# Performance work log

Measured on AMD Instinct MI355X. Metric: run time of the kernel, lower is better.

The kernel has to match this reference:

```python
import jax, jax.numpy as jnp
from jax import lax
import numpy as np

K = 3  # kernel size per dim, dimension=6 -> 3**6 = 729 taps
OFFS = np.stack(np.meshgrid(*([np.arange(K)] * 6), indexing='ij'), axis=-1).reshape(-1, 6).astype(np.int32)


def conv6d(x, kernel):
    """Dense emulation of a 1->1 channel MinkowskiConvolution over 6 spatial dims.

    x: (b, s, s, d, d, d, d) with zeros at absent sparse coordinates.
    kernel: (729,) flattened 3^6 kernel (in=out=1 channel, no bias).
    Zeros at absent coordinates contribute nothing to the gathered sums, so the
    dense conv equals the sparse conv evaluated everywhere.
    """
    xp = jnp.pad(x, [(0, 0)] + [(1, 1)] * 6)
    offs = jnp.asarray(OFFS)
    zero = jnp.int32(0)

    def body(acc, ow):
        off, wt = ow
        sl = lax.dynamic_slice(
            xp, (zero, off[0], off[1], off[2], off[3], off[4], off[5]), x.shape)
        return acc + wt * sl, None

    acc, _ = lax.scan(jax.checkpoint(body), jnp.zeros_like(x), (offs, kernel))
    return acc


def _transpose6d(t):
    # swap the two scale dims and the two image-coordinate pairs:
    # (b, s1, s2, h1, w1, h2, w2) -> (b, s2, s1, h2, w2, h1, w1)
    return jnp.transpose(t, (0, 2, 1, 5, 6, 3, 4))


def setup_inputs() -> dict:
    key = jax.random.key(0)
    k1, k2 = jax.random.split(key)
    x = jax.random.normal(k1, (1, 2, 2, 32, 32, 32, 32), dtype=jnp.float32)
    kernel = jax.random.normal(k2, (K ** 6,), dtype=jnp.float32) * 0.05
    return {"x": x, "kernel": kernel}


def reference(x, kernel):
    # MinkowskiConvolution outputs at the input coordinate set; MinkowskiSigmoid
    # acts on features at those coordinates; to_dense() zero-fills elsewhere.
    # Dense equivalent: mask to the input nonzero set.
    mask = (x != 0).astype(x.dtype)
    branch = lambda z: jax.nn.sigmoid(conv6d(jax.nn.relu(z), kernel))
    # symmetric mode: conv(x) + T(conv(T(x))); T(coords(T(x))) == coords(x)
    y = mask * (branch(x) + _transpose6d(branch(_transpose6d(x))))
    b, s1, s2, d1, d2, d3, d4 = y.shape
    y = y.reshape(b, s1 * s2, d1, d2, d3, d4).sum(axis=1)  # (b, h1, w1, h2, w2)
    return y
```

## Files before the change

kernel.cpp:

```cpp
#include <hip/hip_runtime.h>

typedef _Float16 half8 __attribute__((ext_vector_type(8)));
typedef float f16v __attribute__((ext_vector_type(16)));
typedef float f4 __attribute__((ext_vector_type(4)));
typedef unsigned long long ull;

#define X_SLAB   1048576
#define PLANE_BYTES (34*36*4*2)
#define RPT_SITES (34*34*34*36)
#define RPT_OFF  65536
#define RPT_SLACK 4096
#define TAB_N    (3*6*3*512)
#define TAB_ELEMS  (4*81*8)

__global__ __launch_bounds__(256)
void prep(const float* __restrict__ x, const float* __restrict__ w,
          ull* __restrict__ rpt, _Float16* __restrict__ tabm) {
    unsigned s = blockIdx.x * 256 + threadIdx.x;
    if (s < RPT_SITES) {
        unsigned q = s;
        int j4 = q % 36; q /= 36;
        int j3 = q % 34; q /= 34;
        int j2 = q % 34; q /= 34;
        int j1 = q;
        union { _Float16 h[4]; ull u; } pk;
        pk.u = 0ull;
        if (j1 >= 1 && j1 <= 32 && j2 >= 1 && j2 <= 32 &&
            j3 >= 1 && j3 <= 32 && j4 >= 1 && j4 <= 32) {
            size_t off = (size_t)(j1-1)*32768 + (j2-1)*1024 + (j3-1)*32 + (j4-1);
            #pragma unroll
            for (int t = 0; t < 4; ++t)
                pk.h[t] = (_Float16)fmaxf(x[(size_t)t*X_SLAB + off], 0.f);
        }
        rpt[s] = pk.u;
    }
    if (blockIdx.x == 0) {
        for (int idx = threadIdx.x; idx < TAB_N; idx += 256) {
            int j = idx & 7, l = (idx >> 3) & 63, slice = idx >> 9;
            int p4 = slice % 3, j2rel = (slice/3) % 6, p2 = slice/18;
            int n32 = l & 31;
            int d2 = n32 >> 3, n8 = n32 & 7;
            int k = 8*(l>>5) + j;
            int p5h = k >> 2, t = k & 3;
            int p3 = j2rel - d2;
            float val = 0.f;
            if (p5h < 3 && p3 >= 0 && p3 <= 2) {
                int br = n8 & 1, sc = n8 >> 1, s1 = sc >> 1, s2 = sc & 1;
                int t1 = t >> 1, t2 = t & 1;
                int a = t1 - s1 + 1, b = t2 - s2 + 1;
                int widx = (br == 0)
                    ? (a*243 + b*81 + p2*27 + p3*9 + p4*3 + p5h)
                    : (b*243 + a*81 + p4*27 + p5h*9 + p2*3 + p3);
                val = w[widx];
            }
            tabm[idx] = (_Float16)val;
        }
    }
}

__global__ __launch_bounds__(256)
void conv_mfma(const float* __restrict__ x, const ull* __restrict__ rpt,
               const _Float16* __restrict__ tabm, float* __restrict__ out) {
    __shared__ unsigned char msk[2048];

    const int tid  = threadIdx.x;
    const int lane = tid & 63;
    const int wv   = tid >> 6;
    const int e2b  = blockIdx.x * 4;
    const int e1   = blockIdx.y;
    const int bz   = blockIdx.z;
    const size_t pbase = (size_t)e1*32768 + (size_t)e2b*1024 + (size_t)bz*512;

    {
        int p0 = tid * 8;
        int d2 = p0 >> 9, rem = p0 & 511;
        const float* xb = x + pbase + (size_t)d2*1024 + rem;
        #pragma unroll
        for (int g = 0; g < 2; ++g) {
            f4 a0 = *(const f4*)(xb + (size_t)0*X_SLAB + 4*g);
            f4 a1 = *(const f4*)(xb + (size_t)1*X_SLAB + 4*g);
            f4 a2 = *(const f4*)(xb + (size_t)2*X_SLAB + 4*g);
            f4 a3 = *(const f4*)(xb + (size_t)3*X_SLAB + 4*g);
            unsigned wbits = 0;
            #pragma unroll
            for (int q = 0; q < 4; ++q) {
                unsigned b = (a0[q] != 0.f ? 1u : 0u) | (a1[q] != 0.f ? 2u : 0u)
                           | (a2[q] != 0.f ? 4u : 0u) | (a3[q] != 0.f ? 8u : 0u);
                wbits |= b << (8*q);
            }
            *(unsigned*)&msk[p0 + 4*g] = wbits;
        }
    }
    __syncthreads();

    f16v acc[4];
    #pragma unroll
    for (int r = 0; r < 4; ++r)
        #pragma unroll
        for (int i = 0; i < 16; ++i) acc[r][i] = 0.f;

    const int R   = bz*16 + wv*4;
    const int j4b = (lane & 31) + 2*(lane >> 5);
    const char* awave = (const char*)rpt + (size_t)(R*36 + j4b)*8;

    #pragma unroll 1
    for (int p2 = 0; p2 < 3; ++p2) {
        #pragma unroll 2
        for (int j2 = 0; j2 < 6; ++j2) {
            const int it = p2*6 + j2;
            const char* aptr = awave + ((size_t)(e1+p2)*34 + (e2b+j2))*PLANE_BYTES;
            const _Float16* tb = tabm + it*1536 + lane*8;
            half8 B0 = *(const half8*)(tb);
            half8 B1 = *(const half8*)(tb + 512);
            half8 B2 = *(const half8*)(tb + 1024);
            union { ull u[2]; half8 h; } A[6];
            #pragma unroll
            for (int j3l = 0; j3l < 6; ++j3l) {
                const ull* ap = (const ull*)(aptr + j3l*288);
                A[j3l].u[0] = ap[0];
                A[j3l].u[1] = ap[1];
            }
            #pragma unroll
            for (int j3l = 0; j3l < 6; ++j3l) {
                if (j3l <= 3)
                    acc[j3l]   = __builtin_amdgcn_mfma_f32_32x32x16_f16(A[j3l].h, B0, acc[j3l],   0,0,0);
                if (j3l >= 1 && j3l <= 4)
                    acc[j3l-1] = __builtin_amdgcn_mfma_f32_32x32x16_f16(A[j3l].h, B1, acc[j3l-1], 0,0,0);
                if (j3l >= 2)
                    acc[j3l-2] = __builtin_amdgcn_mfma_f32_32x32x16_f16(A[j3l].h, B2, acc[j3l-2], 0,0,0);
            }
        }
    }

    const int n8 = lane & 7;
    const int d2 = (lane >> 3) & 3;
    const int h  = lane >> 5;
    const int sbit = n8 >> 1;
    float* outp = out + pbase + (size_t)d2*1024;
    #pragma unroll
    for (int rloc = 0; rloc < 4; ++rloc) {
        const int e3loc = wv*4 + rloc;
        float v[16];
        #pragma unroll
        for (int g = 0; g < 4; ++g) {
            unsigned mw = *(const unsigned*)&msk[d2*512 + e3loc*32 + 8*g + 4*h];
            #pragma unroll
            for (int j = 0; j < 4; ++j) {
                float a  = acc[rloc][4*g + j];
                float sg = __builtin_amdgcn_rcpf(1.f + __expf(-a));
                v[4*g+j] = ((mw >> (8*j + sbit)) & 1u) ? sg : 0.f;
            }
        }
        #pragma unroll
        for (int i = 0; i < 16; ++i) {
            v[i] += __shfl_xor(v[i], 1);
            v[i] += __shfl_xor(v[i], 2);
            v[i] += __shfl_xor(v[i], 4);
        }
        if (n8 == 0) {
            #pragma unroll
            for (int g = 0; g < 4; ++g) {
                f4 o; o.x = v[4*g]; o.y = v[4*g+1]; o.z = v[4*g+2]; o.w = v[4*g+3];
                *(f4*)(outp + e3loc*32 + 8*g + 4*h) = o;
            }
        }
    }
}

__global__ void build_wtab(const float* __restrict__ w, float* __restrict__ tab) {
    int idx = blockIdx.x * blockDim.x + threadIdx.x;
    if (idx >= TAB_ELEMS) return;
    int n  = idx & 7;
    int r  = idx >> 3;
    int p5 = r % 3; r /= 3;
    int p4 = r % 3; r /= 3;
    int p3 = r % 3; r /= 3;
    int p2 = r % 3; r /= 3;
    int t  = r;
    int t1 = t >> 1, t2 = t & 1;
    int br = n & 1;
    int s  = n >> 1;
    int s1 = s >> 1, s2 = s & 1;
    int a = t1 - s1 + 1;
    int b = t2 - s2 + 1;
    int widx = (br == 0)
        ? (a*243 + b*81 + p2*27 + p3*9 + p4*3 + p5)
        : (b*243 + a*81 + p4*27 + p5*9 + p2*3 + p3);
    tab[idx] = w[widx];
}

__global__ __launch_bounds__(256)
void conv_fp32(const float* __restrict__ x,
               const float* __restrict__ tab,
               float* __restrict__ out) {
    const int e4 = threadIdx.x;
    const int e3 = blockIdx.x * 8 + threadIdx.y;
    const int e2 = blockIdx.y;
    const int e1 = blockIdx.z;

    float acc[8];
    #pragma unroll
    for (int n = 0; n < 8; ++n) acc[n] = 0.f;

    #pragma unroll 1
    for (int t = 0; t < 4; ++t) {
        const float* st  = x + (size_t)t * X_SLAB;
        const float* wt0 = tab + t * 648;
        #pragma unroll
        for (int p2 = 0; p2 < 3; ++p2) {
            #pragma unroll
            for (int p3 = 0; p3 < 3; ++p3) {
                int i1 = e1 + p2 - 1, i2 = e2 + p3 - 1;
                bool v12 = ((unsigned)i1 < 32u) && ((unsigned)i2 < 32u);
                const float* base = st + (i1*32768 + i2*1024 + (e3-1)*32 + (e4-1));
                const float* wt = wt0 + (p2*3 + p3) * 72;
                #pragma unroll
                for (int p4 = 0; p4 < 3; ++p4) {
                    int i3 = e3 + p4 - 1;
                    bool v3 = v12 && ((unsigned)i3 < 32u);
                    #pragma unroll
                    for (int p5 = 0; p5 < 3; ++p5) {
                        int i4 = e4 + p5 - 1;
                        bool ok = v3 && ((unsigned)i4 < 32u);
                        float v = ok ? fmaxf(base[p4*32 + p5], 0.f) : 0.f;
                        const float* w8 = wt + (p4*3 + p5)*8;
                        #pragma unroll
                        for (int n = 0; n < 8; ++n)
                            acc[n] = fmaf(w8[n], v, acc[n]);
                    }
                }
            }
        }
    }

    const size_t eflat = (size_t)e1*32768 + e2*1024 + e3*32 + e4;
    float res = 0.f;
    #pragma unroll
    for (int i = 0; i < 4; ++i) {
        float xv = x[(size_t)i * X_SLAB + eflat];
        float s0 = __builtin_amdgcn_rcpf(1.f + __expf(-acc[2*i]));
        float s1 = __builtin_amdgcn_rcpf(1.f + __expf(-acc[2*i+1]));
        float m  = (xv != 0.f) ? 1.f : 0.f;
        res = fmaf(m, s0 + s1, res);
    }
    out[eflat] = res;
}

extern "C" void kernel_launch(void* const* d_in, const int* in_sizes, int n_in,
                              void* d_out, int out_size, void* d_ws, size_t ws_size,
                              hipStream_t stream) {
    const float* x = (const float*)d_in[0];
    const float* w = (const float*)d_in[1];
    float* out = (float*)d_out;

    const size_t need = (size_t)RPT_OFF + (size_t)RPT_SITES*8ull + RPT_SLACK;

    if (ws_size >= need) {
        _Float16* tabm = (_Float16*)d_ws;
        ull*      rpt  = (ull*)((char*)d_ws + RPT_OFF);
        prep<<<dim3((RPT_SITES + 255)/256), dim3(256), 0, stream>>>(x, w, rpt, tabm);
        dim3 grd(8, 32, 2), blk(256, 1, 1);
        conv_mfma<<<grd, blk, 0, stream>>>(x, rpt, tabm, out);
    } else {
        float* tab = (float*)d_ws;
        build_wtab<<<dim3((TAB_ELEMS + 255)/256), dim3(256), 0, stream>>>(w, tab);
        dim3 blk(32, 8, 1), grd(4, 32, 32);
        conv_fp32<<<grd, blk, 0, stream>>>(x, tab, out);
    }
}
```

Baseline: 104.8 us.

## Double-buffer A-operand tiles through LDS with async global_load_lds prefetch

Each wave now stages the next iteration's A-operand rows into a per-wave double-buffered LDS slot using global_load_lds, and prefetches the B table into registers one iteration ahead. Manual vmcnt waits let the current iteration's MFMAs overlap with the next iteration's global loads. This hides global load latency but adds LDS traffic and shared memory, which may lower occupancy. It relies on hand-counted vmcnt values and has no wave barrier, which is fragile if the compiler reorders or adds memory ops. The final iteration redundantly restages the last tile.

```diff
diff --git a/kernel.cpp b/kernel.cpp
--- a/kernel.cpp
+++ b/kernel.cpp
@@ -61,6 +61,7 @@
 __global__ __launch_bounds__(256)
 void conv_mfma(const float* __restrict__ x, const ull* __restrict__ rpt,
                const _Float16* __restrict__ tabm, float* __restrict__ out) {
+    __shared__ __align__(16) unsigned char stg[4][2][2048];
     __shared__ unsigned char msk[2048];
 
     const int tid  = threadIdx.x;
@@ -99,36 +100,67 @@
         #pragma unroll
         for (int i = 0; i < 16; ++i) acc[r][i] = 0.f;
 
-    const int R   = bz*16 + wv*4;
-    const int j4b = (lane & 31) + 2*(lane >> 5);
-    const char* awave = (const char*)rpt + (size_t)(R*36 + j4b)*8;
+    const int R     = bz*16 + wv*4;
+    const int j4off = (lane & 31)*8 + (lane >> 5)*16;
+    const char* aglob0 = (const char*)rpt + (size_t)R*288 + lane*16;
+
+    auto stage_to = [&](int it, int slot) {
+        int p2 = it / 6, j2 = it - p2*6;
+        const char* src = aglob0 + ((size_t)(e1+p2)*34 + (e2b+j2))*PLANE_BYTES;
+        unsigned char* dst = &stg[wv][slot][0] + lane*16;
+        #pragma unroll
+        for (int k = 0; k < 2; ++k)
+            __builtin_amdgcn_global_load_lds(
+                (const __attribute__((address_space(1))) unsigned int*)(src + k*1024),
+                (__attribute__((address_space(3))) unsigned int*)(dst + k*1024),
+                16, 0, 0);
+    };
+    auto loadB = [&](int it, half8* B) {
+        const _Float16* tb = tabm + it*1536 + lane*8;
+        B[0] = *(const half8*)(tb);
+        B[1] = *(const half8*)(tb + 512);
+        B[2] = *(const half8*)(tb + 1024);
+    };
+    auto compute = [&](int slot, const half8* B) {
+        const unsigned char* sb = &stg[wv][slot][0];
+        union { ull u[2]; half8 h; } A[6];
+        #pragma unroll
+        for (int j3l = 0; j3l < 6; ++j3l) {
+            const ull* ap = (const ull*)(sb + j3l*288 + j4off);
+            A[j3l].u[0] = ap[0];
+            A[j3l].u[1] = ap[1];
+        }
+        #pragma unroll
+        for (int j3l = 0; j3l < 6; ++j3l) {
+            if (j3l <= 3)
+                acc[j3l]   = __builtin_amdgcn_mfma_f32_32x32x16_f16(A[j3l].h, B[0], acc[j3l],   0,0,0);
+            if (j3l >= 1 && j3l <= 4)
+                acc[j3l-1] = __builtin_amdgcn_mfma_f32_32x32x16_f16(A[j3l].h, B[1], acc[j3l-1], 0,0,0);
+            if (j3l >= 2)
+                acc[j3l-2] = __builtin_amdgcn_mfma_f32_32x32x16_f16(A[j3l].h, B[2], acc[j3l-2], 0,0,0);
+        }
+    };
+
+    half8 Ba[3], Bb[3];
+    stage_to(0, 0);
+    loadB(0, Ba);
 
     #pragma unroll 1
-    for (int p2 = 0; p2 < 3; ++p2) {
-        #pragma unroll 2
-        for (int j2 = 0; j2 < 6; ++j2) {
-            const int it = p2*6 + j2;
-            const char* aptr = awave + ((size_t)(e1+p2)*34 + (e2b+j2))*PLANE_BYTES;
-            const _Float16* tb = tabm + it*1536 + lane*8;
-            half8 B0 = *(const half8*)(tb);
-            half8 B1 = *(const half8*)(tb + 512);
-            half8 B2 = *(const half8*)(tb + 1024);
-            union { ull u[2]; half8 h; } A[6];
-            #pragma unroll
-            for (int j3l = 0; j3l < 6; ++j3l) {
-                const ull* ap = (const ull*)(aptr + j3l*288);
-                A[j3l].u[0] = ap[0];
-                A[j3l].u[1] = ap[1];
-            }
-            #pragma unroll
-            for (int j3l = 0; j3l < 6; ++j3l) {
-                if (j3l <= 3)
-                    acc[j3l]   = __builtin_amdgcn_mfma_f32_32x32x16_f16(A[j3l].h, B0, acc[j3l],   0,0,0);
-                if (j3l >= 1 && j3l <= 4)
-                    acc[j3l-1] = __builtin_amdgcn_mfma_f32_32x32x16_f16(A[j3l].h, B1, acc[j3l-1], 0,0,0);
-                if (j3l >= 2)
-                    acc[j3l-2] = __builtin_amdgcn_mfma_f32_32x32x16_f16(A[j3l].h, B2, acc[j3l-2], 0,0,0);
-            }
+    for (int ip = 0; ip < 9; ++ip) {
+        const int itE = 2*ip;
+        {
+            int nit = itE + 1;
+            stage_to(nit, 1);
+            loadB(nit, Bb);
+            asm volatile("s_waitcnt vmcnt(5)" ::: "memory");
+            compute(0, Ba);
+        }
+        {
+            int nit = (itE + 2 < 18) ? itE + 2 : 17;
+            stage_to(nit, 0);
+            loadB(nit, Ba);
+            asm volatile("s_waitcnt vmcnt(5)" ::: "memory");
+            compute(1, Bb);
         }
     }
 
```

After: 97.69 us. 1.07x faster.
